# Performance work log

Hardware: AMD Instinct MI355X
Metric: run time of the kernel (lower is better)

Reference implementation:

```python
import jax, jax.numpy as jnp
import numpy as np

B, X_DIM, Z_DIM, K, H = 8192, 784, 10, 2000, 300


def setup_inputs() -> dict:
    key = jax.random.key(0)
    ks = jax.random.split(key, 16)

    def lin(k, fan_in, fan_out):
        return jax.random.normal(k, (fan_in, fan_out), jnp.float32) / np.float32(np.sqrt(fan_in))

    return {
        "x": jax.random.uniform(ks[0], (B, X_DIM), jnp.float32),
        "eps": jax.random.normal(ks[1], (B, Z_DIM), jnp.float32),
        # GMM prior params: (1, 2K, Z_DIM), scaled as in torch init
        "z_pre": jax.random.normal(ks[2], (1, 2 * K, Z_DIM), jnp.float32) / np.float32(np.sqrt(K * Z_DIM)),
        # encoder MLP 784 -> 300 -> 300 -> 2*z_dim
        "ew1": lin(ks[3], X_DIM, H), "eb1": jnp.zeros((H,), jnp.float32),
        "ew2": lin(ks[4], H, H),     "eb2": jnp.zeros((H,), jnp.float32),
        "ew3": lin(ks[5], H, 2 * Z_DIM), "eb3": jnp.zeros((2 * Z_DIM,), jnp.float32),
        # decoder MLP z_dim -> 300 -> 300 -> 784
        "dw1": lin(ks[6], Z_DIM, H), "db1": jnp.zeros((H,), jnp.float32),
        "dw2": lin(ks[7], H, H),     "db2": jnp.zeros((H,), jnp.float32),
        "dw3": lin(ks[8], H, X_DIM), "db3": jnp.zeros((X_DIM,), jnp.float32),
    }


def _log_normal(z, m, v):
    # sum over last dim of elementwise Gaussian log-density
    return -0.5 * jnp.sum(jnp.log(2.0 * jnp.pi * v) + (z - m) ** 2 / v, axis=-1)


def reference(x, eps, z_pre, ew1, eb1, ew2, eb2, ew3, eb3, dw1, db1, dw2, db2, dw3, db3):
    elu = jax.nn.elu
    # encoder -> q(z|x) params (gaussian_parameters: split + softplus variance)
    h = elu(x @ ew1 + eb1)
    h = elu(h @ ew2 + eb2)
    h = h @ ew3 + eb3
    qm, qh = jnp.split(h, 2, axis=-1)
    qv = jax.nn.softplus(qh) + 1e-8
    # reparameterized sample
    z = qm + jnp.sqrt(qv) * eps                      # (B, Z)
    # decoder -> Bernoulli logits
    d = elu(z @ dw1 + db1)
    d = elu(d @ dw2 + db2)
    logits = d @ dw3 + db3                            # (B, X)
    # log p(x|z), per image (sum over pixels)
    log_px = jnp.sum(x * logits - jax.nn.softplus(logits), axis=-1)   # (B,)
    # GMM prior: z_pre (1, 2K, Z) -> means/vars (1, K, Z)
    pm, ph = jnp.split(z_pre, 2, axis=1)
    pv = jax.nn.softplus(ph) + 1e-8
    log_qz = _log_normal(z, qm, qv)                                   # (B,)
    # broadcast z vs K components: (B, K, Z) intermediate -> logsumexp
    comp = _log_normal(z[:, None, :], pm, pv)                         # (B, K)
    log_pz = jax.scipy.special.logsumexp(comp, axis=-1) - jnp.log(jnp.float32(K))
    kl_iw = log_qz - log_pz                                           # (B,)
    nelbo = jnp.mean(-log_px + kl_iw)
    kl = jnp.mean(kl_iw)
    rec = jnp.mean(-log_px)
    return jnp.stack([nelbo, kl, rec])
```

## Files before the change

kernel.cpp:

```cpp
#include <hip/hip_runtime.h>
#include <hip/hip_bf16.h>
#include <hip/hip_fp8.h>
#include <math.h>

#define BB 8192
#define XD 784
#define ZD 10
#define KK 2000
#define HH 300

typedef unsigned char uchar16 __attribute__((ext_vector_type(16)));
typedef long lng2 __attribute__((ext_vector_type(2)));
typedef float f32x4 __attribute__((ext_vector_type(4)));

__device__ __forceinline__ float sp_(float x) {
    return fmaxf(x, 0.f) + __logf(1.f + __expf(-fabsf(x)));
}
__device__ __forceinline__ float elu_(float x) { return x > 0.f ? x : __expf(x) - 1.f; }
__device__ __forceinline__ unsigned char f8_(float v) {
    __hip_fp8_e4m3 t(v);
    return (unsigned char)t.__x;
}
__device__ __forceinline__ uchar16 ld16_(const unsigned char* p) {
    return *reinterpret_cast<const uchar16*>(p);
}
__device__ __forceinline__ void mm64(f32x4& acc, uchar16 a, uchar16 b) {
    lng2 la = __builtin_bit_cast(lng2, a);
    lng2 lb = __builtin_bit_cast(lng2, b);
    acc = __builtin_amdgcn_mfma_f32_16x16x32_fp8_fp8(la[0], lb[0], acc, 0, 0, 0);
    acc = __builtin_amdgcn_mfma_f32_16x16x32_fp8_fp8(la[1], lb[1], acc, 0, 0, 0);
}
__device__ __forceinline__ int fpi_(int chunk, int row, int k) {
    return ((chunk + (k >> 6)) * 64 + row + (((k >> 3) & 3) << 4)) * 16
           + (k & 7) + (((k >> 5) & 1) << 3);
}

template<int LMODE, int KP, int NI, bool AG>
__device__ __forceinline__ void layerRf(
    const int tid,
    const unsigned char* __restrict__ actin,
    const unsigned char* __restrict__ Wt,
    const float* __restrict__ bias,
    unsigned char* __restrict__ actout,
    float* __restrict__ c3L, float* __restrict__ redL,
    const float* __restrict__ xrow, float INV, float OUTS)
{
    const int w = tid >> 6, l = tid & 63;
    const int wl = w & 7, wh = w >> 3;
    const int cl = l & 15, hi = l >> 4, g4 = hi << 2;
    constexpr int KS = KP / 64;
    constexpr int NJ = (NI + 1) / 2;
    constexpr int NP = (NJ + 1) / 2;
    const unsigned char* bsrc = Wt + l * 16;

    float rA[2][4];
    #pragma unroll
    for (int rg = 0; rg < 2; ++rg)
        #pragma unroll
        for (int rr = 0; rr < 4; ++rr) rA[rg][rr] = 0.f;

    #pragma unroll
    for (int p = 0; p < NP; ++p) {
        f32x4 acc[2][2];
        #pragma unroll
        for (int j = 0; j < 2; ++j)
            #pragma unroll
            for (int rg = 0; rg < 2; ++rg) acc[j][rg] = (f32x4){0.f, 0.f, 0.f, 0.f};

        int niC[2], rawv[2];
        #pragma unroll
        for (int j = 0; j < 2; ++j) {
            const int njIdx = 2 * p + j;
            const int raw = (njIdx < NJ) ? (2 * njIdx + wh) : (NI - 1);
            rawv[j] = (njIdx < NJ) ? (2 * njIdx + wh) : NI;
            niC[j] = (raw < NI) ? raw : (NI - 1);
        }

        uchar16 Bb[2][2], Ab[2][2];
        #pragma unroll
        for (int j = 0; j < 2; ++j)
            Bb[0][j] = ld16_(bsrc + (((size_t)(niC[j] * 8 + wl) * KS) << 10));
        if constexpr (AG) {
            #pragma unroll
            for (int rg = 0; rg < 2; ++rg)
                Ab[0][rg] = ld16_(actin + ((rg * KS) * 64 + l) * 16);
        }

        #pragma unroll
        for (int ki = 0; ki < KS; ++ki) {
            const int cur = ki & 1, nxt = cur ^ 1;
            if (ki + 1 < KS) {
                #pragma unroll
                for (int j = 0; j < 2; ++j)
                    Bb[nxt][j] = ld16_(bsrc + (((size_t)(niC[j] * 8 + wl) * KS + ki + 1) << 10));
                if constexpr (AG) {
                    #pragma unroll
                    for (int rg = 0; rg < 2; ++rg)
                        Ab[nxt][rg] = ld16_(actin + ((rg * KS + ki + 1) * 64 + l) * 16);
                }
            }
            uchar16 a[2];
            if constexpr (AG) {
                a[0] = Ab[cur][0]; a[1] = Ab[cur][1];
            } else {
                a[0] = ld16_(actin + ((0 * KS + ki) * 64 + l) * 16);
                a[1] = ld16_(actin + ((1 * KS + ki) * 64 + l) * 16);
            }
            #pragma unroll
            for (int j = 0; j < 2; ++j)
                #pragma unroll
                for (int rg = 0; rg < 2; ++rg)
                    mm64(acc[j][rg], a[rg], Bb[cur][j]);
        }

        #pragma unroll
        for (int j = 0; j < 2; ++j) {
            const bool act = rawv[j] < NI;
            const int c = rawv[j] * 128 + wl * 16 + cl;
            if constexpr (LMODE == 0) {
                const float bb = (act && c < HH) ? bias[c] : 0.f;
                #pragma unroll
                for (int rg = 0; rg < 2; ++rg)
                    #pragma unroll
                    for (int rr = 0; rr < 4; ++rr) {
                        float o = (c < HH) ? elu_(acc[j][rg][rr] * INV + bb) : 0.f;
                        if (act && c < 320)
                            actout[fpi_(rg * 5, g4 + rr, c)] = f8_(o * OUTS);
                    }
            } else if constexpr (LMODE == 1) {
                const int cc = wl * 16 + cl;
                if (act && cc < 20) {
                    #pragma unroll
                    for (int rg = 0; rg < 2; ++rg)
                        #pragma unroll
                        for (int rr = 0; rr < 4; ++rr)
                            c3L[(rg * 16 + g4 + rr) * 24 + cc] = acc[j][rg][rr] * INV + bias[cc];
                }
            } else {
                if (act && c < XD) {
                    const float bb = bias[c];
                    #pragma unroll
                    for (int rg = 0; rg < 2; ++rg)
                        #pragma unroll
                        for (int rr = 0; rr < 4; ++rr) {
                            float lv = acc[j][rg][rr] * INV + bb;
                            float xv = xrow[(size_t)(rg * 16 + g4 + rr) * XD + c];
                            rA[rg][rr] += xv * lv - sp_(lv);
                        }
                }
            }
        }
    }

    if constexpr (LMODE == 2) {
        #pragma unroll
        for (int rg = 0; rg < 2; ++rg)
            #pragma unroll
            for (int rr = 0; rr < 4; ++rr) {
                float s = rA[rg][rr];
                s += __shfl_xor(s, 1); s += __shfl_xor(s, 2);
                s += __shfl_xor(s, 4); s += __shfl_xor(s, 8);
                if (cl == 0) redL[(rg * 16 + g4 + rr) * 16 + w] = s;
            }
    }
}

__device__ __forceinline__ void layerCf(
    const int tid,
    const unsigned char* __restrict__ fbL,
    const unsigned char* __restrict__ G,
    const float* __restrict__ cbias,
    float* __restrict__ redM, float* __restrict__ redS)
{
    const int w = tid >> 6, l = tid & 63;
    const int wl = w & 7, wh = w >> 3;
    const int cl = l & 15, hi = l >> 4, g4 = hi << 2;
    const unsigned char* bsrc = G + l * 16;

    uchar16 a[2];
    a[0] = ld16_(fbL + (0 * 64 + l) * 16);
    a[1] = ld16_(fbL + (1 * 64 + l) * 16);

    float rA[2][4], rB[2][4];
    #pragma unroll
    for (int rg = 0; rg < 2; ++rg)
        #pragma unroll
        for (int rr = 0; rr < 4; ++rr) { rA[rg][rr] = -1e30f; rB[rg][rr] = 0.f; }

    uchar16 c0 = ld16_(bsrc + (((size_t)(wh * 8 + wl)) << 10));
    #pragma unroll
    for (int nj = 0; nj < 8; ++nj) {
        uchar16 p0 = c0;
        if (nj + 1 < 8)
            p0 = ld16_(bsrc + (((size_t)((2 * (nj + 1) + wh) * 8 + wl)) << 10));
        const int c = ((2 * nj + wh) * 8 + wl) * 16 + cl;
        const float cb = cbias[c];
        f32x4 acc[2];
        #pragma unroll
        for (int rg = 0; rg < 2; ++rg) {
            acc[rg] = (f32x4){0.f, 0.f, 0.f, 0.f};
            mm64(acc[rg], a[rg], c0);
        }
        #pragma unroll
        for (int rg = 0; rg < 2; ++rg)
            #pragma unroll
            for (int rr = 0; rr < 4; ++rr) {
                float v = acc[rg][rr] * (1.f / 256.f) + cb;
                float mx = fmaxf(v, rA[rg][rr]);
                rB[rg][rr] = rB[rg][rr] * __expf(rA[rg][rr] - mx) + __expf(v - mx);
                rA[rg][rr] = mx;
            }
        c0 = p0;
    }
    #pragma unroll
    for (int d = 1; d <= 8; d <<= 1)
        #pragma unroll
        for (int rg = 0; rg < 2; ++rg)
            #pragma unroll
            for (int rr = 0; rr < 4; ++rr) {
                float mo = __shfl_xor(rA[rg][rr], d);
                float so = __shfl_xor(rB[rg][rr], d);
                float M = fmaxf(rA[rg][rr], mo);
                rB[rg][rr] = rB[rg][rr] * __expf(rA[rg][rr] - M) + so * __expf(mo - M);
                rA[rg][rr] = M;
            }
    if (cl == 0) {
        #pragma unroll
        for (int rg = 0; rg < 2; ++rg)
            #pragma unroll
            for (int rr = 0; rr < 4; ++rr) {
                redM[(rg * 16 + g4 + rr) * 16 + w] = rA[rg][rr];
                redS[(rg * 16 + g4 + rr) * 16 + w] = rB[rg][rr];
            }
    }
}

__global__ __launch_bounds__(1024, 1)
void fused_k(const float* __restrict__ xg,
             const unsigned char* __restrict__ xg2,
             const unsigned char* __restrict__ w1t, const float* __restrict__ eb1,
             const unsigned char* __restrict__ w2t, const float* __restrict__ eb2,
             const unsigned char* __restrict__ w3t, const float* __restrict__ eb3,
             const unsigned char* __restrict__ d1t, const float* __restrict__ db1,
             const unsigned char* __restrict__ d2t, const float* __restrict__ db2,
             const unsigned char* __restrict__ d3t, const float* __restrict__ db3,
             const unsigned char* __restrict__ G, const float* __restrict__ cbias,
             const float* __restrict__ eps, float* __restrict__ part)
{
    __shared__ __align__(16) unsigned char actP[10240];
    __shared__ __align__(16) unsigned char actQ[10240];
    __shared__ __align__(16) unsigned char fbL[2048];
    __shared__ float uredc[1568];

    float* c3L  = uredc;
    float* redM = uredc;
    float* redS = uredc + 512;
    float* redL = uredc + 1024;
    float* lqzL = uredc + 1536;

    const int tid = threadIdx.x;
    const int m0 = blockIdx.x * 32;
    const unsigned char* Aslab = xg2 + (size_t)blockIdx.x * 26624;

    if (tid < 128) reinterpret_cast<uint4*>(fbL)[tid] = (uint4){0u, 0u, 0u, 0u};
    __syncthreads();

    layerRf<0, 832, 3, true>(tid, Aslab, w1t, eb1, actP, nullptr, nullptr, nullptr,
                             1.f / 1024.f, 16.f);
    __syncthreads();
    layerRf<0, 320, 3, false>(tid, actP, w2t, eb2, actQ, nullptr, nullptr, nullptr,
                              1.f / 1024.f, 16.f);
    __syncthreads();
    layerRf<1, 320, 1, false>(tid, actQ, w3t, eb3, nullptr, c3L, nullptr, nullptr,
                              1.f / 1024.f, 0.f);
    __syncthreads();

    if (tid < 32) {
        float a = 0.f;
        const int rg = tid >> 4, rl = tid & 15;
        #pragma unroll
        for (int j = 0; j < ZD; ++j) {
            float qm = c3L[tid * 24 + j];
            float qh = c3L[tid * 24 + 10 + j];
            float qv = sp_(qh) + 1e-8f;
            float e  = eps[(size_t)(m0 + tid) * ZD + j];
            float zj = qm + sqrtf(qv) * e;
            fbL[fpi_(rg, rl, j)]      = f8_(zj * zj * 4.f);
            fbL[fpi_(rg, rl, 10 + j)] = f8_(zj * 4.f);
            float d = zj - qm;
            a += __logf(6.283185307179586f * qv) + d * d / qv;
        }
        lqzL[tid] = -0.5f * a;
    }
    __syncthreads();

    layerRf<0, 64, 3, false>(tid, fbL, d1t, db1, actP, nullptr, nullptr, nullptr,
                             1.f / 64.f, 16.f);
    __syncthreads();
    layerRf<0, 320, 3, false>(tid, actP, d2t, db2, actQ, nullptr, nullptr, nullptr,
                              1.f / 1024.f, 16.f);
    __syncthreads();
    layerRf<2, 320, 7, false>(tid, actQ, d3t, db3, nullptr, nullptr, redL,
                              xg + (size_t)m0 * XD, 1.f / 1024.f, 0.f);
    __syncthreads();
    layerCf(tid, fbL, G, cbias, redM, redS);
    __syncthreads();

    if (tid < 32) {
        float M = -1e30f, S = 0.f;
        #pragma unroll
        for (int w16 = 0; w16 < 16; ++w16) {
            float m = redM[tid * 16 + w16], s = redS[tid * 16 + w16];
            float M2 = fmaxf(M, m);
            S = S * __expf(M - M2) + s * __expf(m - M2);
            M = M2;
        }
        float lpz = M + __logf(S) - 7.6009024595420824f;
        float lpx = 0.f;
        #pragma unroll
        for (int w16 = 0; w16 < 16; ++w16) lpx += redL[tid * 16 + w16];
        float kl = lqzL[tid] - lpz;
        float ne = kl - lpx, re = -lpx;
        #pragma unroll
        for (int d = 1; d <= 16; d <<= 1) {
            ne += __shfl_xor(ne, d); kl += __shfl_xor(kl, d); re += __shfl_xor(re, d);
        }
        if (tid == 0) {
            part[blockIdx.x * 3 + 0] = ne;
            part[blockIdx.x * 3 + 1] = kl;
            part[blockIdx.x * 3 + 2] = re;
        }
    }
}

__global__ __launch_bounds__(256)
void prep_k(const float* __restrict__ x,
            const float* __restrict__ ew1, const float* __restrict__ ew2,
            const float* __restrict__ ew3, const float* __restrict__ dw1,
            const float* __restrict__ dw2, const float* __restrict__ dw3,
            const float* __restrict__ zpre,
            unsigned char* __restrict__ w1t, unsigned char* __restrict__ w2t,
            unsigned char* __restrict__ w3t, unsigned char* __restrict__ d1t,
            unsigned char* __restrict__ d2t, unsigned char* __restrict__ d3t,
            unsigned char* __restrict__ G, float* __restrict__ cbias,
            unsigned char* __restrict__ xg2)
{
    const int t = blockIdx.x * 256 + threadIdx.x;
    const int y = blockIdx.y;
    const int lane = t & 63, chunk = t >> 6;
    const int cl = lane & 15, hi = lane >> 4;

    auto genw = [&](const float* W, unsigned char* out, int NT, int KS,
                    int K, int N, float s) {
        if (chunk >= NT * KS) return;
        const int kc = chunk % KS, nt = chunk / KS;
        const int n = nt * 16 + cl;
        uchar16 v;
        #pragma unroll
        for (int e = 0; e < 16; ++e) {
            const int k = kc * 64 + (e >> 3) * 32 + hi * 8 + (e & 7);
            v[e] = f8_((n < N && k < K) ? W[(size_t)k * N + n] * s : 0.f);
        }
        *reinterpret_cast<uchar16*>(&out[(size_t)t * 16]) = v;
    };

    if (y == 0) genw(ew1, w1t, 24, 13, XD, HH, 64.f);
    else if (y == 1) genw(ew2, w2t, 24, 5, HH, HH, 64.f);
    else if (y == 2) genw(ew3, w3t, 8, 5, HH, 2 * ZD, 64.f);
    else if (y == 3) {
        if (chunk >= 24) return;
        const int nt = chunk;
        const int n = nt * 16 + cl;
        uchar16 v;
        #pragma unroll
        for (int e = 0; e < 16; ++e) {
            const int k = (e >> 3) * 32 + hi * 8 + (e & 7);
            float vv = (n < HH && k >= 10 && k < 20) ? dw1[(size_t)(k - 10) * HH + n] * 16.f : 0.f;
            v[e] = f8_(vv);
        }
        *reinterpret_cast<uchar16*>(&d1t[(size_t)t * 16]) = v;
    }
    else if (y == 4) genw(dw2, d2t, 24, 5, HH, HH, 64.f);
    else if (y == 5) genw(dw3, d3t, 56, 5, HH, XD, 64.f);
    else if (y == 6) {
        if (chunk >= 128) return;
        const int nt = chunk;
        const int n = nt * 16 + cl;
        uchar16 v;
        #pragma unroll
        for (int e = 0; e < 16; ++e) {
            const int k = (e >> 3) * 32 + hi * 8 + (e & 7);
            float vv = 0.f;
            if (n < KK) {
                if (k < 10) {
                    float h = zpre[(KK + n) * ZD + k];
                    float vr = sp_(h) + 1e-8f;
                    vv = (-0.5f / vr) * 64.f;
                } else if (k < 20) {
                    float m = zpre[n * ZD + (k - 10)];
                    float h = zpre[(KK + n) * ZD + (k - 10)];
                    float vr = sp_(h) + 1e-8f;
                    vv = (m / vr) * 64.f;
                }
            }
            v[e] = f8_(vv);
        }
        *reinterpret_cast<uchar16*>(&G[(size_t)t * 16]) = v;
        if (hi == 0) {
            float cb = -1e30f;
            if (n < KK) {
                float csum = 0.f;
                #pragma unroll
                for (int j = 0; j < ZD; ++j) {
                    float m = zpre[n * ZD + j];
                    float h = zpre[(KK + n) * ZD + j];
                    float vr = sp_(h) + 1e-8f;
                    csum += __logf(6.283185307179586f * vr) + m * m / vr;
                }
                cb = -0.5f * csum;
            }
            cbias[n] = cb;
        }
    } else {
        if (chunk >= 256 * 26) return;
        const int kc = chunk % 13;
        const int rg = (chunk / 13) & 1;
        const int slab = chunk / 26;
        const int row = slab * 32 + rg * 16 + cl;
        uchar16 v;
        #pragma unroll
        for (int half = 0; half < 2; ++half) {
            const int kb = kc * 64 + half * 32 + hi * 8;
            float f[8];
            if (kb + 7 < XD) {
                float4 f0 = *reinterpret_cast<const float4*>(&x[(size_t)row * XD + kb]);
                float4 f1 = *reinterpret_cast<const float4*>(&x[(size_t)row * XD + kb + 4]);
                f[0] = f0.x; f[1] = f0.y; f[2] = f0.z; f[3] = f0.w;
                f[4] = f1.x; f[5] = f1.y; f[6] = f1.z; f[7] = f1.w;
            } else {
                #pragma unroll
                for (int e = 0; e < 8; ++e) f[e] = 0.f;
            }
            #pragma unroll
            for (int e = 0; e < 8; ++e) v[half * 8 + e] = f8_(f[e] * 16.f);
        }
        *reinterpret_cast<uchar16*>(&xg2[(size_t)t * 16]) = v;
    }
}

__global__ void fin_k(const float* __restrict__ part, float* __restrict__ out)
{
    int c = threadIdx.x >> 6, l = threadIdx.x & 63;
    if (c < 3) {
        float s = 0.f;
        for (int i = l; i < 256; i += 64) s += part[i * 3 + c];
        #pragma unroll
        for (int d = 1; d < 64; d <<= 1) s += __shfl_xor(s, d);
        if (l == 0) out[c] = s / (float)BB;
    }
}

extern "C" void kernel_launch(void* const* d_in, const int* in_sizes, int n_in,
                              void* d_out, int out_size, void* d_ws, size_t ws_size,
                              hipStream_t stream)
{
    const float* x    = (const float*)d_in[0];
    const float* eps  = (const float*)d_in[1];
    const float* zpre = (const float*)d_in[2];
    const float* ew1  = (const float*)d_in[3];
    const float* eb1  = (const float*)d_in[4];
    const float* ew2  = (const float*)d_in[5];
    const float* eb2  = (const float*)d_in[6];
    const float* ew3  = (const float*)d_in[7];
    const float* eb3  = (const float*)d_in[8];
    const float* dw1  = (const float*)d_in[9];
    const float* db1  = (const float*)d_in[10];
    const float* dw2  = (const float*)d_in[11];
    const float* db2  = (const float*)d_in[12];
    const float* dw3  = (const float*)d_in[13];
    const float* db3  = (const float*)d_in[14];
    float* out = (float*)d_out;

    float* ws    = (float*)d_ws;
    float* part  = ws;
    float* cbias = part + 768;
    unsigned char* ub = (unsigned char*)(cbias + 2048);
    unsigned char* xg2 = ub; ub += (size_t)256 * 26624;
    unsigned char* w1t = ub; ub += 24 * 13 * 1024;
    unsigned char* w2t = ub; ub += 24 * 5 * 1024;
    unsigned char* w3t = ub; ub += 8 * 5 * 1024;
    unsigned char* d1t = ub; ub += 24 * 1 * 1024;
    unsigned char* d2t = ub; ub += 24 * 5 * 1024;
    unsigned char* d3t = ub; ub += 56 * 5 * 1024;
    unsigned char* G   = ub; ub += 128 * 1 * 1024;

    dim3 blk(256);
    prep_k<<<dim3(1664, 8), blk, 0, stream>>>(x, ew1, ew2, ew3, dw1, dw2, dw3, zpre,
                                              w1t, w2t, w3t, d1t, d2t, d3t, G, cbias, xg2);
    fused_k<<<256, 1024, 0, stream>>>(x, xg2, w1t, eb1, w2t, eb2, w3t, eb3,
                                      d1t, db1, d2t, db2, d3t, db3, G, cbias, eps, part);
    fin_k<<<1, 256, 0, stream>>>(part, out);
}
```

Baseline: 57.46 us.

## Quantize x to fp8 inside fused kernel shared memory instead of prep pass

Removes the prep-kernel pass that converted x to fp8 into a global workspace slab. Each fused block now reads its 32 rows of fp32 x, converts them to fp8, and stores them in a 26 KB shared buffer that the first layer reads. This drops a global write and read of the quantized input and shrinks the prep grid. It also skips loads and MFMAs for padded column tiles (njIdx >= NJ), at the cost of more LDS per block and the conversion work sitting on the fused kernel's critical path.

```diff
diff --git a/kernel.cpp b/kernel.cpp
--- a/kernel.cpp
+++ b/kernel.cpp
@@ -35,7 +35,7 @@
            + (k & 7) + (((k >> 5) & 1) << 3);
 }
 
-template<int LMODE, int KP, int NI, bool AG>
+template<int LMODE, int KP, int NI>
 __device__ __forceinline__ void layerRf(
     const int tid,
     const unsigned char* __restrict__ actin,
@@ -76,15 +76,11 @@
             niC[j] = (raw < NI) ? raw : (NI - 1);
         }
 
-        uchar16 Bb[2][2], Ab[2][2];
+        uchar16 Bb[2][2];
         #pragma unroll
         for (int j = 0; j < 2; ++j)
-            Bb[0][j] = ld16_(bsrc + (((size_t)(niC[j] * 8 + wl) * KS) << 10));
-        if constexpr (AG) {
-            #pragma unroll
-            for (int rg = 0; rg < 2; ++rg)
-                Ab[0][rg] = ld16_(actin + ((rg * KS) * 64 + l) * 16);
-        }
+            if ((2 * p + j) < NJ)
+                Bb[0][j] = ld16_(bsrc + (((size_t)(niC[j] * 8 + wl) * KS) << 10));
 
         #pragma unroll
         for (int ki = 0; ki < KS; ++ki) {
@@ -92,29 +88,23 @@
             if (ki + 1 < KS) {
                 #pragma unroll
                 for (int j = 0; j < 2; ++j)
-                    Bb[nxt][j] = ld16_(bsrc + (((size_t)(niC[j] * 8 + wl) * KS + ki + 1) << 10));
-                if constexpr (AG) {
+                    if ((2 * p + j) < NJ)
+                        Bb[nxt][j] = ld16_(bsrc + (((size_t)(niC[j] * 8 + wl) * KS + ki + 1) << 10));
+            }
+            uchar16 a[2];
+            a[0] = ld16_(actin + ((0 * KS + ki) * 64 + l) * 16);
+            a[1] = ld16_(actin + ((1 * KS + ki) * 64 + l) * 16);
+            #pragma unroll
+            for (int j = 0; j < 2; ++j)
+                if ((2 * p + j) < NJ)
                     #pragma unroll
                     for (int rg = 0; rg < 2; ++rg)
-                        Ab[nxt][rg] = ld16_(actin + ((rg * KS + ki + 1) * 64 + l) * 16);
-                }
-            }
-            uchar16 a[2];
-            if constexpr (AG) {
-                a[0] = Ab[cur][0]; a[1] = Ab[cur][1];
-            } else {
-                a[0] = ld16_(actin + ((0 * KS + ki) * 64 + l) * 16);
-                a[1] = ld16_(actin + ((1 * KS + ki) * 64 + l) * 16);
-            }
-            #pragma unroll
-            for (int j = 0; j < 2; ++j)
-                #pragma unroll
-                for (int rg = 0; rg < 2; ++rg)
-                    mm64(acc[j][rg], a[rg], Bb[cur][j]);
+                        mm64(acc[j][rg], a[rg], Bb[cur][j]);
         }
 
         #pragma unroll
         for (int j = 0; j < 2; ++j) {
+            if ((2 * p + j) >= NJ) continue;
             const bool act = rawv[j] < NI;
             const int c = rawv[j] * 128 + wl * 16 + cl;
             if constexpr (LMODE == 0) {
@@ -237,7 +227,6 @@
 
 __global__ __launch_bounds__(1024, 1)
 void fused_k(const float* __restrict__ xg,
-             const unsigned char* __restrict__ xg2,
              const unsigned char* __restrict__ w1t, const float* __restrict__ eb1,
              const unsigned char* __restrict__ w2t, const float* __restrict__ eb2,
              const unsigned char* __restrict__ w3t, const float* __restrict__ eb3,
@@ -247,6 +236,7 @@
              const unsigned char* __restrict__ G, const float* __restrict__ cbias,
              const float* __restrict__ eps, float* __restrict__ part)
 {
+    __shared__ __align__(16) unsigned char xsf8[26624];
     __shared__ __align__(16) unsigned char actP[10240];
     __shared__ __align__(16) unsigned char actQ[10240];
     __shared__ __align__(16) unsigned char fbL[2048];
@@ -260,19 +250,48 @@
 
     const int tid = threadIdx.x;
     const int m0 = blockIdx.x * 32;
-    const unsigned char* Aslab = xg2 + (size_t)blockIdx.x * 26624;
-
+
+    #pragma unroll
+    for (int it = 0; it < 2; ++it) {
+        const int c = tid + it * 1024;
+        if (c < 26 * 64) {
+            const int chunk = c >> 6, lane = c & 63;
+            const int rg = chunk / 13, kc = chunk % 13;
+            const int row = m0 + rg * 16 + (lane & 15);
+            const int h2 = lane >> 4;
+            uchar16 v;
+            #pragma unroll
+            for (int half = 0; half < 2; ++half) {
+                const int kb = kc * 64 + half * 32 + h2 * 8;
+                if (kb + 7 < XD) {
+                    float4 f0 = *reinterpret_cast<const float4*>(&xg[(size_t)row * XD + kb]);
+                    float4 f1 = *reinterpret_cast<const float4*>(&xg[(size_t)row * XD + kb + 4]);
+                    v[half * 8 + 0] = f8_(f0.x * 16.f); v[half * 8 + 1] = f8_(f0.y * 16.f);
+                    v[half * 8 + 2] = f8_(f0.z * 16.f); v[half * 8 + 3] = f8_(f0.w * 16.f);
+                    v[half * 8 + 4] = f8_(f1.x * 16.f); v[half * 8 + 5] = f8_(f1.y * 16.f);
+                    v[half * 8 + 6] = f8_(f1.z * 16.f); v[half * 8 + 7] = f8_(f1.w * 16.f);
+                } else {
+                    #pragma unroll
+                    for (int e = 0; e < 8; ++e) {
+                        const int k = kb + e;
+                        v[half * 8 + e] = (k < XD) ? f8_(xg[(size_t)row * XD + k] * 16.f) : (unsigned char)0;
+                    }
+                }
+            }
+            *reinterpret_cast<uchar16*>(&xsf8[c * 16]) = v;
+        }
+    }
     if (tid < 128) reinterpret_cast<uint4*>(fbL)[tid] = (uint4){0u, 0u, 0u, 0u};
     __syncthreads();
 
-    layerRf<0, 832, 3, true>(tid, Aslab, w1t, eb1, actP, nullptr, nullptr, nullptr,
-                             1.f / 1024.f, 16.f);
-    __syncthreads();
-    layerRf<0, 320, 3, false>(tid, actP, w2t, eb2, actQ, nullptr, nullptr, nullptr,
-                              1.f / 1024.f, 16.f);
-    __syncthreads();
-    layerRf<1, 320, 1, false>(tid, actQ, w3t, eb3, nullptr, c3L, nullptr, nullptr,
-                              1.f / 1024.f, 0.f);
+    layerRf<0, 832, 3>(tid, xsf8, w1t, eb1, actP, nullptr, nullptr, nullptr,
+                       1.f / 1024.f, 16.f);
+    __syncthreads();
+    layerRf<0, 320, 3>(tid, actP, w2t, eb2, actQ, nullptr, nullptr, nullptr,
+                       1.f / 1024.f, 16.f);
+    __syncthreads();
+    layerRf<1, 320, 1>(tid, actQ, w3t, eb3, nullptr, c3L, nullptr, nullptr,
+                       1.f / 1024.f, 0.f);
     __syncthreads();
 
     if (tid < 32) {
@@ -294,14 +313,14 @@
     }
     __syncthreads();
 
-    layerRf<0, 64, 3, false>(tid, fbL, d1t, db1, actP, nullptr, nullptr, nullptr,
-                             1.f / 64.f, 16.f);
-    __syncthreads();
-    layerRf<0, 320, 3, false>(tid, actP, d2t, db2, actQ, nullptr, nullptr, nullptr,
-                              1.f / 1024.f, 16.f);
-    __syncthreads();
-    layerRf<2, 320, 7, false>(tid, actQ, d3t, db3, nullptr, nullptr, redL,
-                              xg + (size_t)m0 * XD, 1.f / 1024.f, 0.f);
+    layerRf<0, 64, 3>(tid, fbL, d1t, db1, actP, nullptr, nullptr, nullptr,
+                      1.f / 64.f, 16.f);
+    __syncthreads();
+    layerRf<0, 320, 3>(tid, actP, d2t, db2, actQ, nullptr, nullptr, nullptr,
+                       1.f / 1024.f, 16.f);
+    __syncthreads();
+    layerRf<2, 320, 7>(tid, actQ, d3t, db3, nullptr, nullptr, redL,
+                       xg + (size_t)m0 * XD, 1.f / 1024.f, 0.f);
     __syncthreads();
     layerCf(tid, fbL, G, cbias, redM, redS);
     __syncthreads();
@@ -334,16 +353,14 @@
 }
 
 __global__ __launch_bounds__(256)
-void prep_k(const float* __restrict__ x,
-            const float* __restrict__ ew1, const float* __restrict__ ew2,
+void prep_k(const float* __restrict__ ew1, const float* __restrict__ ew2,
             const float* __restrict__ ew3, const float* __restrict__ dw1,
             const float* __restrict__ dw2, const float* __restrict__ dw3,
             const float* __restrict__ zpre,
             unsigned char* __restrict__ w1t, unsigned char* __restrict__ w2t,
             unsigned char* __restrict__ w3t, unsigned char* __restrict__ d1t,
             unsigned char* __restrict__ d2t, unsigned char* __restrict__ d3t,
-            unsigned char* __restrict__ G, float* __restrict__ cbias,
-            unsigned char* __restrict__ xg2)
+            unsigned char* __restrict__ G, float* __restrict__ cbias)
 {
     const int t = blockIdx.x * 256 + threadIdx.x;
     const int y = blockIdx.y;
@@ -369,8 +386,7 @@
     else if (y == 2) genw(ew3, w3t, 8, 5, HH, 2 * ZD, 64.f);
     else if (y == 3) {
         if (chunk >= 24) return;
-        const int nt = chunk;
-        const int n = nt * 16 + cl;
+        const int n = chunk * 16 + cl;
         uchar16 v;
         #pragma unroll
         for (int e = 0; e < 16; ++e) {
@@ -382,10 +398,9 @@
     }
     else if (y == 4) genw(dw2, d2t, 24, 5, HH, HH, 64.f);
     else if (y == 5) genw(dw3, d3t, 56, 5, HH, XD, 64.f);
-    else if (y == 6) {
+    else {
         if (chunk >= 128) return;
-        const int nt = chunk;
-        const int n = nt * 16 + cl;
+        const int n = chunk * 16 + cl;
         uchar16 v;
         #pragma unroll
         for (int e = 0; e < 16; ++e) {
@@ -421,30 +436,6 @@
             }
             cbias[n] = cb;
         }
-    } else {
-        if (chunk >= 256 * 26) return;
-        const int kc = chunk % 13;
-        const int rg = (chunk / 13) & 1;
-        const int slab = chunk / 26;
-        const int row = slab * 32 + rg * 16 + cl;
-        uchar16 v;
-        #pragma unroll
-        for (int half = 0; half < 2; ++half) {
-            const int kb = kc * 64 + half * 32 + hi * 8;
-            float f[8];
-            if (kb + 7 < XD) {
-                float4 f0 = *reinterpret_cast<const float4*>(&x[(size_t)row * XD + kb]);
-                float4 f1 = *reinterpret_cast<const float4*>(&x[(size_t)row * XD + kb + 4]);
-                f[0] = f0.x; f[1] = f0.y; f[2] = f0.z; f[3] = f0.w;
-                f[4] = f1.x; f[5] = f1.y; f[6] = f1.z; f[7] = f1.w;
-            } else {
-                #pragma unroll
-                for (int e = 0; e < 8; ++e) f[e] = 0.f;
-            }
-            #pragma unroll
-            for (int e = 0; e < 8; ++e) v[half * 8 + e] = f8_(f[e] * 16.f);
-        }
-        *reinterpret_cast<uchar16*>(&xg2[(size_t)t * 16]) = v;
     }
 }
 
@@ -485,7 +476,6 @@
     float* part  = ws;
     float* cbias = part + 768;
     unsigned char* ub = (unsigned char*)(cbias + 2048);
-    unsigned char* xg2 = ub; ub += (size_t)256 * 26624;
     unsigned char* w1t = ub; ub += 24 * 13 * 1024;
     unsigned char* w2t = ub; ub += 24 * 5 * 1024;
     unsigned char* w3t = ub; ub += 8 * 5 * 1024;
@@ -495,9 +485,9 @@
     unsigned char* G   = ub; ub += 128 * 1 * 1024;
 
     dim3 blk(256);
-    prep_k<<<dim3(1664, 8), blk, 0, stream>>>(x, ew1, ew2, ew3, dw1, dw2, dw3, zpre,
-                                              w1t, w2t, w3t, d1t, d2t, d3t, G, cbias, xg2);
-    fused_k<<<256, 1024, 0, stream>>>(x, xg2, w1t, eb1, w2t, eb2, w3t, eb3,
+    prep_k<<<dim3(78, 7), blk, 0, stream>>>(ew1, ew2, ew3, dw1, dw2, dw3, zpre,
+                                            w1t, w2t, w3t, d1t, d2t, d3t, G, cbias);
+    fused_k<<<256, 1024, 0, stream>>>(x, w1t, eb1, w2t, eb2, w3t, eb3,
                                       d1t, db1, d2t, db2, d3t, db3, G, cbias, eps, part);
     fin_k<<<1, 256, 0, stream>>>(part, out);
 }
```

Result: faster. 51.40 us (median of 3 runs) (-10.5%).
